# Optimization experiments

Measured on AMD Instinct MI355X. Metric: run time of the kernel, lower is better.

The kernel has to match this reference:

```python
import jax, jax.numpy as jnp
import numpy as np

N_NODES = 50000
N_EDGES = 800000
D_IN = 128
D_OUT = 128
BN_EPS = 1e-5


def setup_inputs() -> dict:
    key = jax.random.key(0)
    ks = jax.random.split(key, 8)
    node_feats = jax.random.normal(ks[0], (N_NODES, D_IN), dtype=jnp.float32)
    src = jax.random.randint(ks[1], (N_EDGES,), 0, N_NODES, dtype=jnp.int32)
    dst = jax.random.randint(ks[2], (N_EDGES,), 0, N_NODES, dtype=jnp.int32)
    # Glorot-ish init for weights
    scale = 1.0 / np.sqrt(D_IN)
    W = jax.random.normal(ks[3], (D_IN, D_OUT), dtype=jnp.float32) * scale
    b = jnp.zeros((D_OUT,), dtype=jnp.float32)
    Wr = jax.random.normal(ks[4], (D_IN, D_OUT), dtype=jnp.float32) * scale
    br = jnp.zeros((D_OUT,), dtype=jnp.float32)
    gamma = jnp.ones((D_OUT,), dtype=jnp.float32)
    beta = jnp.zeros((D_OUT,), dtype=jnp.float32)
    return {"node_feats": node_feats, "src": src, "dst": dst, "W": W, "b": b,
            "Wr": Wr, "br": br, "gamma": gamma, "beta": beta}


def reference(node_feats, src, dst, W, b, Wr, br, gamma, beta):
    N = node_feats.shape[0]
    ones_e = jnp.ones(src.shape[0], dtype=node_feats.dtype)
    # DGL GraphConv norm='both': D_out^{-1/2} on source side, D_in^{-1/2} on dest side
    deg_out = jnp.clip(jax.ops.segment_sum(ones_e, src, num_segments=N), 1.0)
    deg_in = jnp.clip(jax.ops.segment_sum(ones_e, dst, num_segments=N), 1.0)
    h = node_feats * jax.lax.rsqrt(deg_out)[:, None]        # [N, D_in]
    agg = jax.ops.segment_sum(h[src], dst, num_segments=N)  # gather + scatter-add, [N, D_in]
    agg = agg * jax.lax.rsqrt(deg_in)[:, None]
    gcn = jax.nn.relu(agg @ W + b)                           # GraphConv activation=relu
    res = jax.nn.relu(node_feats @ Wr + br)                  # residual branch
    y = gcn + res
    # BatchNorm1d (training mode: biased batch stats)
    mean = jnp.mean(y, axis=0)
    var = jnp.mean(jnp.square(y - mean), axis=0)
    out = (y - mean) * jax.lax.rsqrt(var + BN_EPS) * gamma + beta
    return out
```

## Files before the change

kernel.cpp:

```cpp
#include <hip/hip_runtime.h>

#define N_NODES 50000
#define N_EDGES 800000
#define D 128
#define BN_EPS 1e-5f
#define AGG_BLOCKS 2048
#define SCAN_BLOCKS 196
#define CHUNKS 64
#define EPC (N_EDGES / CHUNKS)
#define HALF_BINS 25600
#define HALF_U32 12800

typedef short bf16x8 __attribute__((ext_vector_type(8)));
typedef float f32x4  __attribute__((ext_vector_type(4)));
typedef unsigned int u32x4 __attribute__((ext_vector_type(4)));


__device__ __forceinline__ unsigned int pack_rne(float a, float b) {
    unsigned int ua = __float_as_uint(a); ua += 0x7fffu + ((ua >> 16) & 1u);
    unsigned int ub = __float_as_uint(b); ub += 0x7fffu + ((ub >> 16) & 1u);
    return (ua >> 16) | (ub & 0xffff0000u);
}
__device__ __forceinline__ unsigned short pack1_rne(float a) {
    unsigned int ua = __float_as_uint(a); ua += 0x7fffu + ((ua >> 16) & 1u);
    return (unsigned short)(ua >> 16);
}

__global__ __launch_bounds__(256) void hist_kernel(
        const int* __restrict__ dst, const int* __restrict__ src,
        unsigned int* __restrict__ histD, unsigned int* __restrict__ histS,
        const float* __restrict__ W, const float* __restrict__ Wr,
        uint4* __restrict__ pW, uint4* __restrict__ pWr) {
    __shared__ unsigned int h[HALF_U32];
    int tid = threadIdx.x;
    int c = blockIdx.x, r = blockIdx.y;
    if (c >= CHUNKS) {
        if (r != 0 || blockIdx.z != 0) return;
        int t = (c - CHUNKS) * 256 + tid;
        const float* S = (t & 2048) ? Wr : W;
        uint4* Dst     = (t & 2048) ? pWr : pW;
        int e = t & 2047;
        int lane = e & 63, ks = (e >> 6) & 3, ct = e >> 8;
        int n  = ct * 16 + (lane & 15);
        int k0 = ks * 32 + (lane >> 4) * 8;
        float v[8];
        #pragma unroll
        for (int j = 0; j < 8; j++) v[j] = S[(k0 + j) * D + n];
        uint4 rr;
        rr.x = pack_rne(v[0], v[1]); rr.y = pack_rne(v[2], v[3]);
        rr.z = pack_rne(v[4], v[5]); rr.w = pack_rne(v[6], v[7]);
        Dst[e] = rr;
        return;
    }
    const int* keys = blockIdx.z ? src : dst;
    unsigned int* hist = blockIdx.z ? histS : histD;
    for (int j = tid; j < HALF_U32; j += 256) h[j] = 0u;
    __syncthreads();
    int base = c * EPC;
    int lo = r * HALF_BINS;
    for (int i = tid; i < EPC; i += 256) {
        int b = keys[base + i] - lo;
        if ((unsigned)b < (unsigned)HALF_BINS)
            atomicAdd(&h[b >> 1], 1u << ((b & 1) * 16));
    }
    __syncthreads();
    unsigned int* out = hist + ((size_t)(r * CHUNKS + c)) * HALF_U32;
    for (int j = tid; j < HALF_U32; j += 256) out[j] = h[j];
}

__global__ __launch_bounds__(256) void merge_kernel(
        unsigned int* __restrict__ histD, unsigned int* __restrict__ histS,
        int* __restrict__ cnt_in, int* __restrict__ cnt_out) {
    int q = blockIdx.x * 256 + threadIdx.x;
    int r = blockIdx.y;
    unsigned int* hist = blockIdx.z ? histS : histD;
    int* cnt = blockIdx.z ? cnt_out : cnt_in;
    unsigned int lo = 0, hi = 0;
    for (int c = 0; c < CHUNKS; c++) {
        size_t idx = ((size_t)(r * CHUNKS + c)) * HALF_U32 + q;
        unsigned int v = hist[idx];
        hist[idx] = lo | (hi << 16);
        lo += v & 0xffffu; hi += v >> 16;
    }
    int n0 = r * HALF_BINS + q * 2;
    cnt[n0]     = (int)lo;
    cnt[n0 + 1] = (int)hi;
}

__global__ __launch_bounds__(256) void scan1_kernel(
        const int* __restrict__ cnt_in, int* __restrict__ row_ptr, int* __restrict__ blk_sum) {
    __shared__ int sh[256];
    int t = threadIdx.x;
    int i = blockIdx.x * 256 + t;
    int v = cnt_in[i];
    sh[t] = v;
    __syncthreads();
    int inc = v;
    #pragma unroll
    for (int off = 1; off < 256; off <<= 1) {
        int u = (t >= off) ? sh[t - off] : 0;
        __syncthreads();
        inc += u; sh[t] = inc;
        __syncthreads();
    }
    row_ptr[i] = inc - v;
    if (t == 255) blk_sum[blockIdx.x] = inc;
}

__global__ __launch_bounds__(256) void scan3_kernel(
        const int* __restrict__ cnt_in, const int* __restrict__ cnt_out,
        const int* __restrict__ blk_sum, int* __restrict__ row_ptr,
        float* __restrict__ rin, float* __restrict__ rout) {
    __shared__ int sh[256];
    int t = threadIdx.x;
    int v = (t < SCAN_BLOCKS) ? blk_sum[t] : 0;
    sh[t] = v;
    __syncthreads();
    int inc = v;
    #pragma unroll
    for (int off = 1; off < 256; off <<= 1) {
        int u = (t >= off) ? sh[t - off] : 0;
        __syncthreads();
        inc += u; sh[t] = inc;
        __syncthreads();
    }
    int boff = (blockIdx.x == 0) ? 0 : sh[blockIdx.x - 1];
    int i = blockIdx.x * 256 + t;
    if (i < N_NODES) {
        row_ptr[i] = row_ptr[i] + boff;
        int ci = cnt_in[i], co = cnt_out[i];
        rin[i]  = rsqrtf((float)(ci > 1 ? ci : 1));
        rout[i] = rsqrtf((float)(co > 1 ? co : 1));
    }
    if (blockIdx.x == SCAN_BLOCKS - 1 && t == 0) row_ptr[N_NODES] = N_EDGES;
}

__global__ __launch_bounds__(512) void fill2_kernel(
        const int* __restrict__ src, const int* __restrict__ dst,
        const int* __restrict__ row_ptr, const unsigned int* __restrict__ histP,
        int* __restrict__ csr_src) {
    __shared__ unsigned int h[HALF_U32];
    int tid = threadIdx.x;
    int c = blockIdx.x;
    int base = c * EPC;
    for (int r = 0; r < 2; r++) {
        for (int j = tid; j < HALF_U32; j += 512) h[j] = 0u;
        __syncthreads();
        int lo = r * HALF_BINS;
        const unsigned int* pre_c = histP + ((size_t)(r * CHUNKS + c)) * HALF_U32;
        for (int i = tid; i < EPC; i += 512) {
            int d = dst[base + i];
            int b = d - lo;
            if ((unsigned)b < (unsigned)HALF_BINS) {
                int sh = (b & 1) * 16;
                unsigned int old = atomicAdd(&h[b >> 1], 1u << sh);
                unsigned int rank = (old >> sh) & 0xffffu;
                unsigned int pre = (pre_c[b >> 1] >> sh) & 0xffffu;
                int p = row_ptr[d] + (int)(pre + rank);
                csr_src[p] = src[base + i];
            }
        }
        __syncthreads();
    }
}

__global__ __launch_bounds__(256) void gemm_mfma(
        const float* __restrict__ x, const uint4* __restrict__ pW,
        const uint4* __restrict__ pWr, const float* __restrict__ br,
        const float* __restrict__ rout, unsigned short* __restrict__ hwb,
        unsigned short* __restrict__ resb) {
    __shared__ unsigned short xs[64][136];
    int tid = threadIdx.x, wid = tid >> 6, lane = tid & 63;
    int quad = lane >> 4, l15 = lane & 15;
    int r0b = blockIdx.x * 64;
    const float4* xg = (const float4*)(x + (size_t)r0b * D);
    int maxidx = (N_NODES - r0b) * (D / 4);
    #pragma unroll
    for (int i = 0; i < 8; i++) {
        int idx = tid + 256 * i;
        float4 v = (idx < maxidx) ? xg[idx] : make_float4(0.f, 0.f, 0.f, 0.f);
        int row = idx >> 5, c0 = (idx & 31) * 4;
        *(unsigned int*)&xs[row][c0]     = pack_rne(v.x, v.y);
        *(unsigned int*)&xs[row][c0 + 2] = pack_rne(v.z, v.w);
    }
    __syncthreads();
    int wrow0 = wid * 16;
    bf16x8 A[4];
    #pragma unroll
    for (int ks = 0; ks < 4; ks++)
        A[ks] = *(const bf16x8*)&xs[wrow0 + l15][ks * 32 + quad * 8];
    f32x4 accW[8], accR[8];
    #pragma unroll
    for (int ct = 0; ct < 8; ct++) { accW[ct] = (f32x4)0.f; accR[ct] = (f32x4)0.f; }
    #pragma unroll
    for (int ct = 0; ct < 8; ct++) {
        #pragma unroll
        for (int ks = 0; ks < 4; ks++) {
            union { bf16x8 v; uint4 u; } Bw, Br2;
            Bw.u  = pW [(ct * 4 + ks) * 64 + lane];
            Br2.u = pWr[(ct * 4 + ks) * 64 + lane];
            accW[ct] = __builtin_amdgcn_mfma_f32_16x16x32_bf16(A[ks], Bw.v,  accW[ct], 0, 0, 0);
            accR[ct] = __builtin_amdgcn_mfma_f32_16x16x32_bf16(A[ks], Br2.v, accR[ct], 0, 0, 0);
        }
    }
    int r0 = r0b + wrow0;
    float ro[4]; int rowok[4];
    #pragma unroll
    for (int reg = 0; reg < 4; reg++) {
        int row = r0 + quad * 4 + reg;
        rowok[reg] = row < N_NODES;
        ro[reg] = rout[rowok[reg] ? row : N_NODES - 1];
    }
    #pragma unroll
    for (int ct = 0; ct < 8; ct++) {
        int c = ct * 16 + l15;
        float brv = br[c];
        #pragma unroll
        for (int reg = 0; reg < 4; reg++) {
            int row = r0 + quad * 4 + reg;
            if (rowok[reg]) {
                hwb [(size_t)row * D + c] = pack1_rne(accW[ct][reg] * ro[reg]);
                resb[(size_t)row * D + c] = pack1_rne(fmaxf(accR[ct][reg] + brv, 0.f));
            }
        }
    }
}

__device__ __forceinline__ float bf_lo(unsigned int v) { return __uint_as_float(v << 16); }
__device__ __forceinline__ float bf_hi(unsigned int v) { return __uint_as_float(v & 0xffff0000u); }

__device__ __forceinline__ void acc8(float* a, const uint4 v) {
    a[0] += bf_lo(v.x); a[1] += bf_hi(v.x);
    a[2] += bf_lo(v.y); a[3] += bf_hi(v.y);
    a[4] += bf_lo(v.z); a[5] += bf_hi(v.z);
    a[6] += bf_lo(v.w); a[7] += bf_hi(v.w);
}
__device__ __forceinline__ void acc8m(float* a, const uint4 v, float m) {
    a[0] = fmaf(m, bf_lo(v.x), a[0]); a[1] = fmaf(m, bf_hi(v.x), a[1]);
    a[2] = fmaf(m, bf_lo(v.y), a[2]); a[3] = fmaf(m, bf_hi(v.y), a[3]);
    a[4] = fmaf(m, bf_lo(v.z), a[4]); a[5] = fmaf(m, bf_hi(v.z), a[5]);
    a[6] = fmaf(m, bf_lo(v.w), a[6]); a[7] = fmaf(m, bf_hi(v.w), a[7]);
}

__device__ __forceinline__ int sel4(int qg, int i0, int i1, int i2, int i3) {
    int a = (qg & 1) ? i1 : i0;
    int b = (qg & 1) ? i3 : i2;
    return (qg & 2) ? b : a;
}

__device__ __forceinline__ void gather_accum(
        const unsigned int* __restrict__ hwb, int myidx, int cnt,
        int qg, int ql, float* a) {
    int i = 0;
    for (; i + 16 <= cnt; i += 16) {
        int p0 = sel4(qg, __builtin_amdgcn_readlane(myidx, i + 0),
                          __builtin_amdgcn_readlane(myidx, i + 1),
                          __builtin_amdgcn_readlane(myidx, i + 2),
                          __builtin_amdgcn_readlane(myidx, i + 3));
        int p1 = sel4(qg, __builtin_amdgcn_readlane(myidx, i + 4),
                          __builtin_amdgcn_readlane(myidx, i + 5),
                          __builtin_amdgcn_readlane(myidx, i + 6),
                          __builtin_amdgcn_readlane(myidx, i + 7));
        int p2 = sel4(qg, __builtin_amdgcn_readlane(myidx, i + 8),
                          __builtin_amdgcn_readlane(myidx, i + 9),
                          __builtin_amdgcn_readlane(myidx, i + 10),
                          __builtin_amdgcn_readlane(myidx, i + 11));
        int p3 = sel4(qg, __builtin_amdgcn_readlane(myidx, i + 12),
                          __builtin_amdgcn_readlane(myidx, i + 13),
                          __builtin_amdgcn_readlane(myidx, i + 14),
                          __builtin_amdgcn_readlane(myidx, i + 15));
        uint4 v0 = *((const uint4*)(hwb + (size_t)p0 * 64) + ql);
        uint4 v1 = *((const uint4*)(hwb + (size_t)p1 * 64) + ql);
        uint4 v2 = *((const uint4*)(hwb + (size_t)p2 * 64) + ql);
        uint4 v3 = *((const uint4*)(hwb + (size_t)p3 * 64) + ql);
        acc8(a, v0); acc8(a, v1); acc8(a, v2); acc8(a, v3);
    }
    for (; i + 4 <= cnt; i += 4) {
        int p0 = sel4(qg, __builtin_amdgcn_readlane(myidx, i + 0),
                          __builtin_amdgcn_readlane(myidx, i + 1),
                          __builtin_amdgcn_readlane(myidx, i + 2),
                          __builtin_amdgcn_readlane(myidx, i + 3));
        uint4 v0 = *((const uint4*)(hwb + (size_t)p0 * 64) + ql);
        acc8(a, v0);
    }
    int t = cnt - i;
    if (t > 0) {
        int lim = cnt - 1;
        int j1 = i + 1 <= lim ? i + 1 : lim;
        int j2 = i + 2 <= lim ? i + 2 : lim;
        int p0 = sel4(qg, __builtin_amdgcn_readlane(myidx, i),
                          __builtin_amdgcn_readlane(myidx, j1),
                          __builtin_amdgcn_readlane(myidx, j2),
                          __builtin_amdgcn_readlane(myidx, lim));
        uint4 v0 = *((const uint4*)(hwb + (size_t)p0 * 64) + ql);
        float m = (qg < t) ? 1.f : 0.f;
        acc8m(a, v0, m);
    }
}

__global__ __launch_bounds__(256) void agg_kernel(
        const unsigned int* __restrict__ hwb, const int* __restrict__ row_ptr,
        const int* __restrict__ csr_src, const float* __restrict__ rin,
        const float* __restrict__ bias, const unsigned short* __restrict__ resb,
        float* __restrict__ y, float* __restrict__ parts) {
    __shared__ float red[4 * 256];
    int tid = threadIdx.x;
    int lane = tid & 63, wid = tid >> 6;
    int wave = blockIdx.x * 4 + wid;
    int nw = AGG_BLOCKS * 4;
    int qg = lane >> 4;
    int ql = lane & 15;
    float s1[8] = {0,0,0,0,0,0,0,0}, s2[8] = {0,0,0,0,0,0,0,0};
    float4 bv0, bv1;
    if (lane < 16) {
        bv0 = ((const float4*)bias)[2 * lane];
        bv1 = ((const float4*)bias)[2 * lane + 1];
    }
    int n = wave;
    int e0 = 0, e1 = 0, mi = 0;
    u32x4 rv4 = (u32x4)0u;
    float ri = 0.f;
    if (n < N_NODES) {
        e0 = row_ptr[n]; e1 = row_ptr[n + 1];
        ri = rin[n];
        if (lane < 16) rv4 = __builtin_nontemporal_load((const u32x4*)(resb + (size_t)n * D) + lane);
        int c0 = e1 - e0; if (c0 > 64) c0 = 64;
        mi = (lane < c0) ? __builtin_nontemporal_load(csr_src + e0 + lane) : 0;
    }
    while (n < N_NODES) {
        int nn = n + nw;
        int ne0 = 0, ne1 = 0, nmi = 0;
        u32x4 nrv = (u32x4)0u;
        float nri = 0.f;
        if (nn < N_NODES) {
            ne0 = row_ptr[nn]; ne1 = row_ptr[nn + 1];
            nri = rin[nn];
            if (lane < 16) nrv = __builtin_nontemporal_load((const u32x4*)(resb + (size_t)nn * D) + lane);
            int nc = ne1 - ne0; if (nc > 64) nc = 64;
            nmi = (lane < nc) ? __builtin_nontemporal_load(csr_src + ne0 + lane) : 0;
        }
        float a[8] = {0,0,0,0,0,0,0,0};
        {
            int cnt = e1 - e0; if (cnt > 64) cnt = 64;
            gather_accum(hwb, mi, cnt, qg, ql, a);
        }
        for (int j0 = e0 + 64; j0 < e1; j0 += 64) {
            int cnt = e1 - j0; if (cnt > 64) cnt = 64;
            int mw = (lane < cnt) ? __builtin_nontemporal_load(csr_src + j0 + lane) : 0;
            gather_accum(hwb, mw, cnt, qg, ql, a);
        }
        #pragma unroll
        for (int k = 0; k < 8; k++) {
            a[k] += __shfl_xor(a[k], 16);
            a[k] += __shfl_xor(a[k], 32);
        }
        if (lane < 16) {
            float o[8];
            o[0] = fmaxf(a[0] * ri + bv0.x, 0.f) + bf_lo(rv4.x);
            o[1] = fmaxf(a[1] * ri + bv0.y, 0.f) + bf_hi(rv4.x);
            o[2] = fmaxf(a[2] * ri + bv0.z, 0.f) + bf_lo(rv4.y);
            o[3] = fmaxf(a[3] * ri + bv0.w, 0.f) + bf_hi(rv4.y);
            o[4] = fmaxf(a[4] * ri + bv1.x, 0.f) + bf_lo(rv4.z);
            o[5] = fmaxf(a[5] * ri + bv1.y, 0.f) + bf_hi(rv4.z);
            o[6] = fmaxf(a[6] * ri + bv1.z, 0.f) + bf_lo(rv4.w);
            o[7] = fmaxf(a[7] * ri + bv1.w, 0.f) + bf_hi(rv4.w);
            float4* yv = (float4*)(y + (size_t)n * D);
            yv[2 * lane]     = make_float4(o[0], o[1], o[2], o[3]);
            yv[2 * lane + 1] = make_float4(o[4], o[5], o[6], o[7]);
            #pragma unroll
            for (int k = 0; k < 8; k++) { s1[k] += o[k]; s2[k] += o[k] * o[k]; }
        }
        n = nn; e0 = ne0; e1 = ne1; mi = nmi; rv4 = nrv; ri = nri;
    }
    if (lane < 16) {
        int c0 = lane * 8;
        #pragma unroll
        for (int k = 0; k < 8; k++) {
            red[wid * 256 + c0 + k]       = s1[k];
            red[wid * 256 + 128 + c0 + k] = s2[k];
        }
    }
    __syncthreads();
    if (tid < 256) {
        float v = red[tid] + red[256 + tid] + red[512 + tid] + red[768 + tid];
        parts[(size_t)blockIdx.x * 256 + tid] = v;
    }
}

__global__ __launch_bounds__(256) void bn_fin2(
        const float* __restrict__ parts, const float* __restrict__ gamma,
        const float* __restrict__ beta, float* __restrict__ scsh) {
    __shared__ float rs1[256], rs2[256];
    int c = blockIdx.x, t = threadIdx.x;
    float s1 = 0.f, s2 = 0.f;
    for (int b = t; b < AGG_BLOCKS; b += 256) {
        s1 += parts[(size_t)b * 256 + c];
        s2 += parts[(size_t)b * 256 + 128 + c];
    }
    rs1[t] = s1; rs2[t] = s2;
    __syncthreads();
    for (int off = 128; off > 0; off >>= 1) {
        if (t < off) { rs1[t] += rs1[t + off]; rs2[t] += rs2[t + off]; }
        __syncthreads();
    }
    if (t == 0) {
        const float invN = 1.0f / (float)N_NODES;
        float mean = rs1[0] * invN;
        float var  = rs2[0] * invN - mean * mean;
        float sc = gamma[c] * rsqrtf(var + BN_EPS);
        scsh[c] = sc;
        scsh[128 + c] = beta[c] - mean * sc;
    }
}

__global__ void norm_kernel(float* __restrict__ y, const float* __restrict__ scsh) {
    int i = blockIdx.x * blockDim.x + threadIdx.x;
    if (i < N_NODES * 32) {
        float4 v = ((float4*)y)[i];
        int c = (i & 31) * 4;
        v.x = v.x * scsh[c]     + scsh[128 + c];
        v.y = v.y * scsh[c + 1] + scsh[128 + c + 1];
        v.z = v.z * scsh[c + 2] + scsh[128 + c + 2];
        v.w = v.w * scsh[c + 3] + scsh[128 + c + 3];
        ((float4*)y)[i] = v;
    }
}

extern "C" void kernel_launch(void* const* d_in, const int* in_sizes, int n_in,
                              void* d_out, int out_size, void* d_ws, size_t ws_size,
                              hipStream_t stream) {
    const float* x     = (const float*)d_in[0];
    const int*   src   = (const int*)d_in[1];
    const int*   dst   = (const int*)d_in[2];
    const float* W     = (const float*)d_in[3];
    const float* b     = (const float*)d_in[4];
    const float* Wr    = (const float*)d_in[5];
    const float* br    = (const float*)d_in[6];
    const float* gamma = (const float*)d_in[7];
    const float* beta  = (const float*)d_in[8];
    float* out = (float*)d_out;

    char* ws = (char*)d_ws;
    int*   cnt_in  = (int*)(ws + 0);
    int*   cnt_out = (int*)(ws + 262144);
    int*   row_ptr = (int*)(ws + 524288);
    float* rin     = (float*)(ws + 1048576);
    float* rout    = (float*)(ws + 1310720);
    float* scsh    = (float*)(ws + 1576960);
    int*   blk_sum = (int*)(ws + 1579008);
    int*   csr_src = (int*)(ws + 1581056);
    unsigned short* hwb = (unsigned short*)(ws + 4800000);
    float* parts   = (float*)(ws + 17600000);
    uint4* pW      = (uint4*)(ws + 19697152);
    uint4* pWr     = (uint4*)(ws + 19729920);
    unsigned int* histD = (unsigned int*)(ws + 19762688);
    unsigned int* histS = (unsigned int*)(ws + 26316288);
    unsigned short* resb = (unsigned short*)(ws + 19762688);

    hist_kernel<<<dim3(CHUNKS + 16, 2, 2), 256, 0, stream>>>(dst, src, histD, histS, W, Wr, pW, pWr);
    merge_kernel<<<dim3(HALF_U32 / 256, 2, 2), 256, 0, stream>>>(histD, histS, cnt_in, cnt_out);
    scan1_kernel<<<SCAN_BLOCKS, 256, 0, stream>>>(cnt_in, row_ptr, blk_sum);
    scan3_kernel<<<SCAN_BLOCKS, 256, 0, stream>>>(cnt_in, cnt_out, blk_sum, row_ptr, rin, rout);
    fill2_kernel<<<CHUNKS, 512, 0, stream>>>(src, dst, row_ptr, histD, csr_src);
    gemm_mfma<<<(N_NODES + 63) / 64, 256, 0, stream>>>(x, pW, pWr, br, rout, hwb, resb);
    agg_kernel<<<AGG_BLOCKS, 256, 0, stream>>>((const unsigned int*)hwb, row_ptr, csr_src, rin, b, resb, out, parts);
    bn_fin2<<<128, 256, 0, stream>>>(parts, gamma, beta, scsh);
    norm_kernel<<<(N_NODES * 32 + 255) / 256, 256, 0, stream>>>(out, scsh);
}
```

Before: 239.0 us.

## Store gathered features in FP8, bf16 pre-norm output, and parallelize CSR fill

New measurement: 219.7 us. -8.1%, faster.

```diff
diff --git a/kernel.cpp b/kernel.cpp
--- a/kernel.cpp
+++ b/kernel.cpp
@@ -13,6 +13,7 @@
 
 typedef short bf16x8 __attribute__((ext_vector_type(8)));
 typedef float f32x4  __attribute__((ext_vector_type(4)));
+typedef float f32x2  __attribute__((ext_vector_type(2)));
 typedef unsigned int u32x4 __attribute__((ext_vector_type(4)));
 
 
@@ -24,6 +25,10 @@
 __device__ __forceinline__ unsigned short pack1_rne(float a) {
     unsigned int ua = __float_as_uint(a); ua += 0x7fffu + ((ua >> 16) & 1u);
     return (unsigned short)(ua >> 16);
+}
+__device__ __forceinline__ unsigned char pack1_fp8(float a) {
+    unsigned int u = __builtin_amdgcn_cvt_pk_fp8_f32(a, a, 0, false);
+    return (unsigned char)(u & 0xffu);
 }
 
 __global__ __launch_bounds__(256) void hist_kernel(
@@ -141,33 +146,30 @@
         int* __restrict__ csr_src) {
     __shared__ unsigned int h[HALF_U32];
     int tid = threadIdx.x;
-    int c = blockIdx.x;
+    int c = blockIdx.x, r = blockIdx.y;
     int base = c * EPC;
-    for (int r = 0; r < 2; r++) {
-        for (int j = tid; j < HALF_U32; j += 512) h[j] = 0u;
-        __syncthreads();
-        int lo = r * HALF_BINS;
-        const unsigned int* pre_c = histP + ((size_t)(r * CHUNKS + c)) * HALF_U32;
-        for (int i = tid; i < EPC; i += 512) {
-            int d = dst[base + i];
-            int b = d - lo;
-            if ((unsigned)b < (unsigned)HALF_BINS) {
-                int sh = (b & 1) * 16;
-                unsigned int old = atomicAdd(&h[b >> 1], 1u << sh);
-                unsigned int rank = (old >> sh) & 0xffffu;
-                unsigned int pre = (pre_c[b >> 1] >> sh) & 0xffffu;
-                int p = row_ptr[d] + (int)(pre + rank);
-                csr_src[p] = src[base + i];
-            }
-        }
-        __syncthreads();
+    for (int j = tid; j < HALF_U32; j += 512) h[j] = 0u;
+    __syncthreads();
+    int lo = r * HALF_BINS;
+    const unsigned int* pre_c = histP + ((size_t)(r * CHUNKS + c)) * HALF_U32;
+    for (int i = tid; i < EPC; i += 512) {
+        int d = dst[base + i];
+        int b = d - lo;
+        if ((unsigned)b < (unsigned)HALF_BINS) {
+            int sh = (b & 1) * 16;
+            unsigned int old = atomicAdd(&h[b >> 1], 1u << sh);
+            unsigned int rank = (old >> sh) & 0xffffu;
+            unsigned int pre = (pre_c[b >> 1] >> sh) & 0xffffu;
+            int p = row_ptr[d] + (int)(pre + rank);
+            csr_src[p] = src[base + i];
+        }
     }
 }
 
 __global__ __launch_bounds__(256) void gemm_mfma(
         const float* __restrict__ x, const uint4* __restrict__ pW,
         const uint4* __restrict__ pWr, const float* __restrict__ br,
-        const float* __restrict__ rout, unsigned short* __restrict__ hwb,
+        const float* __restrict__ rout, unsigned char* __restrict__ hwb8,
         unsigned short* __restrict__ resb) {
     __shared__ unsigned short xs[64][136];
     int tid = threadIdx.x, wid = tid >> 6, lane = tid & 63;
@@ -219,7 +221,7 @@
         for (int reg = 0; reg < 4; reg++) {
             int row = r0 + quad * 4 + reg;
             if (rowok[reg]) {
-                hwb [(size_t)row * D + c] = pack1_rne(accW[ct][reg] * ro[reg]);
+                hwb8[(size_t)row * D + c] = pack1_fp8(accW[ct][reg] * ro[reg]);
                 resb[(size_t)row * D + c] = pack1_rne(fmaxf(accR[ct][reg] + brv, 0.f));
             }
         }
@@ -229,17 +231,23 @@
 __device__ __forceinline__ float bf_lo(unsigned int v) { return __uint_as_float(v << 16); }
 __device__ __forceinline__ float bf_hi(unsigned int v) { return __uint_as_float(v & 0xffff0000u); }
 
-__device__ __forceinline__ void acc8(float* a, const uint4 v) {
-    a[0] += bf_lo(v.x); a[1] += bf_hi(v.x);
-    a[2] += bf_lo(v.y); a[3] += bf_hi(v.y);
-    a[4] += bf_lo(v.z); a[5] += bf_hi(v.z);
-    a[6] += bf_lo(v.w); a[7] += bf_hi(v.w);
-}
-__device__ __forceinline__ void acc8m(float* a, const uint4 v, float m) {
-    a[0] = fmaf(m, bf_lo(v.x), a[0]); a[1] = fmaf(m, bf_hi(v.x), a[1]);
-    a[2] = fmaf(m, bf_lo(v.y), a[2]); a[3] = fmaf(m, bf_hi(v.y), a[3]);
-    a[4] = fmaf(m, bf_lo(v.z), a[4]); a[5] = fmaf(m, bf_hi(v.z), a[5]);
-    a[6] = fmaf(m, bf_lo(v.w), a[6]); a[7] = fmaf(m, bf_hi(v.w), a[7]);
+__device__ __forceinline__ void acc8f8(float* a, const uint2 v) {
+    f32x2 p0 = __builtin_amdgcn_cvt_pk_f32_fp8(v.x, false);
+    f32x2 p1 = __builtin_amdgcn_cvt_pk_f32_fp8(v.x, true);
+    f32x2 p2 = __builtin_amdgcn_cvt_pk_f32_fp8(v.y, false);
+    f32x2 p3 = __builtin_amdgcn_cvt_pk_f32_fp8(v.y, true);
+    a[0] += p0.x; a[1] += p0.y; a[2] += p1.x; a[3] += p1.y;
+    a[4] += p2.x; a[5] += p2.y; a[6] += p3.x; a[7] += p3.y;
+}
+__device__ __forceinline__ void acc8f8m(float* a, const uint2 v, float m) {
+    f32x2 p0 = __builtin_amdgcn_cvt_pk_f32_fp8(v.x, false);
+    f32x2 p1 = __builtin_amdgcn_cvt_pk_f32_fp8(v.x, true);
+    f32x2 p2 = __builtin_amdgcn_cvt_pk_f32_fp8(v.y, false);
+    f32x2 p3 = __builtin_amdgcn_cvt_pk_f32_fp8(v.y, true);
+    a[0] = fmaf(m, p0.x, a[0]); a[1] = fmaf(m, p0.y, a[1]);
+    a[2] = fmaf(m, p1.x, a[2]); a[3] = fmaf(m, p1.y, a[3]);
+    a[4] = fmaf(m, p2.x, a[4]); a[5] = fmaf(m, p2.y, a[5]);
+    a[6] = fmaf(m, p3.x, a[6]); a[7] = fmaf(m, p3.y, a[7]);
 }
 
 __device__ __forceinline__ int sel4(int qg, int i0, int i1, int i2, int i3) {
@@ -249,7 +257,7 @@
 }
 
 __device__ __forceinline__ void gather_accum(
-        const unsigned int* __restrict__ hwb, int myidx, int cnt,
+        const unsigned char* __restrict__ hwb8, int myidx, int cnt,
         int qg, int ql, float* a) {
     int i = 0;
     for (; i + 16 <= cnt; i += 16) {
@@ -269,19 +277,19 @@
                           __builtin_amdgcn_readlane(myidx, i + 13),
                           __builtin_amdgcn_readlane(myidx, i + 14),
                           __builtin_amdgcn_readlane(myidx, i + 15));
-        uint4 v0 = *((const uint4*)(hwb + (size_t)p0 * 64) + ql);
-        uint4 v1 = *((const uint4*)(hwb + (size_t)p1 * 64) + ql);
-        uint4 v2 = *((const uint4*)(hwb + (size_t)p2 * 64) + ql);
-        uint4 v3 = *((const uint4*)(hwb + (size_t)p3 * 64) + ql);
-        acc8(a, v0); acc8(a, v1); acc8(a, v2); acc8(a, v3);
+        uint2 v0 = *((const uint2*)(hwb8 + (size_t)p0 * 128) + ql);
+        uint2 v1 = *((const uint2*)(hwb8 + (size_t)p1 * 128) + ql);
+        uint2 v2 = *((const uint2*)(hwb8 + (size_t)p2 * 128) + ql);
+        uint2 v3 = *((const uint2*)(hwb8 + (size_t)p3 * 128) + ql);
+        acc8f8(a, v0); acc8f8(a, v1); acc8f8(a, v2); acc8f8(a, v3);
     }
     for (; i + 4 <= cnt; i += 4) {
         int p0 = sel4(qg, __builtin_amdgcn_readlane(myidx, i + 0),
                           __builtin_amdgcn_readlane(myidx, i + 1),
                           __builtin_amdgcn_readlane(myidx, i + 2),
                           __builtin_amdgcn_readlane(myidx, i + 3));
-        uint4 v0 = *((const uint4*)(hwb + (size_t)p0 * 64) + ql);
-        acc8(a, v0);
+        uint2 v0 = *((const uint2*)(hwb8 + (size_t)p0 * 128) + ql);
+        acc8f8(a, v0);
     }
     int t = cnt - i;
     if (t > 0) {
@@ -292,17 +300,17 @@
                           __builtin_amdgcn_readlane(myidx, j1),
                           __builtin_amdgcn_readlane(myidx, j2),
                           __builtin_amdgcn_readlane(myidx, lim));
-        uint4 v0 = *((const uint4*)(hwb + (size_t)p0 * 64) + ql);
+        uint2 v0 = *((const uint2*)(hwb8 + (size_t)p0 * 128) + ql);
         float m = (qg < t) ? 1.f : 0.f;
-        acc8m(a, v0, m);
+        acc8f8m(a, v0, m);
     }
 }
 
 __global__ __launch_bounds__(256) void agg_kernel(
-        const unsigned int* __restrict__ hwb, const int* __restrict__ row_ptr,
+        const unsigned char* __restrict__ hwb8, const int* __restrict__ row_ptr,
         const int* __restrict__ csr_src, const float* __restrict__ rin,
         const float* __restrict__ bias, const unsigned short* __restrict__ resb,
-        float* __restrict__ y, float* __restrict__ parts) {
+        unsigned short* __restrict__ yb, float* __restrict__ parts) {
     __shared__ float red[4 * 256];
     int tid = threadIdx.x;
     int lane = tid & 63, wid = tid >> 6;
@@ -342,12 +350,12 @@
         float a[8] = {0,0,0,0,0,0,0,0};
         {
             int cnt = e1 - e0; if (cnt > 64) cnt = 64;
-            gather_accum(hwb, mi, cnt, qg, ql, a);
+            gather_accum(hwb8, mi, cnt, qg, ql, a);
         }
         for (int j0 = e0 + 64; j0 < e1; j0 += 64) {
             int cnt = e1 - j0; if (cnt > 64) cnt = 64;
             int mw = (lane < cnt) ? __builtin_nontemporal_load(csr_src + j0 + lane) : 0;
-            gather_accum(hwb, mw, cnt, qg, ql, a);
+            gather_accum(hwb8, mw, cnt, qg, ql, a);
         }
         #pragma unroll
         for (int k = 0; k < 8; k++) {
@@ -364,9 +372,10 @@
             o[5] = fmaxf(a[5] * ri + bv1.y, 0.f) + bf_hi(rv4.z);
             o[6] = fmaxf(a[6] * ri + bv1.z, 0.f) + bf_lo(rv4.w);
             o[7] = fmaxf(a[7] * ri + bv1.w, 0.f) + bf_hi(rv4.w);
-            float4* yv = (float4*)(y + (size_t)n * D);
-            yv[2 * lane]     = make_float4(o[0], o[1], o[2], o[3]);
-            yv[2 * lane + 1] = make_float4(o[4], o[5], o[6], o[7]);
+            uint4 w;
+            w.x = pack_rne(o[0], o[1]); w.y = pack_rne(o[2], o[3]);
+            w.z = pack_rne(o[4], o[5]); w.w = pack_rne(o[6], o[7]);
+            *((uint4*)(yb + (size_t)n * D) + lane) = w;
             #pragma unroll
             for (int k = 0; k < 8; k++) { s1[k] += o[k]; s2[k] += o[k] * o[k]; }
         }
@@ -413,16 +422,23 @@
     }
 }
 
-__global__ void norm_kernel(float* __restrict__ y, const float* __restrict__ scsh) {
+__global__ void norm_kernel(const unsigned short* __restrict__ yb,
+                            const float* __restrict__ scsh, float* __restrict__ out) {
     int i = blockIdx.x * blockDim.x + threadIdx.x;
-    if (i < N_NODES * 32) {
-        float4 v = ((float4*)y)[i];
-        int c = (i & 31) * 4;
-        v.x = v.x * scsh[c]     + scsh[128 + c];
-        v.y = v.y * scsh[c + 1] + scsh[128 + c + 1];
-        v.z = v.z * scsh[c + 2] + scsh[128 + c + 2];
-        v.w = v.w * scsh[c + 3] + scsh[128 + c + 3];
-        ((float4*)y)[i] = v;
+    if (i < N_NODES * 16) {
+        uint4 v = ((const uint4*)yb)[i];
+        int c = (i & 15) * 8;
+        float4 o0, o1;
+        o0.x = bf_lo(v.x) * scsh[c]     + scsh[128 + c];
+        o0.y = bf_hi(v.x) * scsh[c + 1] + scsh[128 + c + 1];
+        o0.z = bf_lo(v.y) * scsh[c + 2] + scsh[128 + c + 2];
+        o0.w = bf_hi(v.y) * scsh[c + 3] + scsh[128 + c + 3];
+        o1.x = bf_lo(v.z) * scsh[c + 4] + scsh[128 + c + 4];
+        o1.y = bf_hi(v.z) * scsh[c + 5] + scsh[128 + c + 5];
+        o1.z = bf_lo(v.w) * scsh[c + 6] + scsh[128 + c + 6];
+        o1.w = bf_hi(v.w) * scsh[c + 7] + scsh[128 + c + 7];
+        float4* ov = (float4*)out + (size_t)i * 2;
+        ov[0] = o0; ov[1] = o1;
     }
 }
 
@@ -444,26 +460,27 @@
     int*   cnt_in  = (int*)(ws + 0);
     int*   cnt_out = (int*)(ws + 262144);
     int*   row_ptr = (int*)(ws + 524288);
-    float* rin     = (float*)(ws + 1048576);
-    float* rout    = (float*)(ws + 1310720);
-    float* scsh    = (float*)(ws + 1576960);
-    int*   blk_sum = (int*)(ws + 1579008);
-    int*   csr_src = (int*)(ws + 1581056);
-    unsigned short* hwb = (unsigned short*)(ws + 4800000);
-    float* parts   = (float*)(ws + 17600000);
-    uint4* pW      = (uint4*)(ws + 19697152);
-    uint4* pWr     = (uint4*)(ws + 19729920);
-    unsigned int* histD = (unsigned int*)(ws + 19762688);
-    unsigned int* histS = (unsigned int*)(ws + 26316288);
-    unsigned short* resb = (unsigned short*)(ws + 19762688);
+    float* rin     = (float*)(ws + 786432);
+    float* rout    = (float*)(ws + 1048576);
+    float* scsh    = (float*)(ws + 1310720);
+    int*   blk_sum = (int*)(ws + 1312768);
+    int*   csr_src = (int*)(ws + 1576960);
+    unsigned char*  hwb8 = (unsigned char*)(ws + 4800000);
+    unsigned short* resb = (unsigned short*)(ws + 11200000);
+    unsigned short* yb   = (unsigned short*)(ws + 24000000);
+    float* parts   = (float*)(ws + 36800000);
+    uint4* pW      = (uint4*)(ws + 38897152);
+    uint4* pWr     = (uint4*)(ws + 38929920);
+    unsigned int* histD = (unsigned int*)(ws + 38962688);
+    unsigned int* histS = (unsigned int*)(ws + 45516288);
 
     hist_kernel<<<dim3(CHUNKS + 16, 2, 2), 256, 0, stream>>>(dst, src, histD, histS, W, Wr, pW, pWr);
     merge_kernel<<<dim3(HALF_U32 / 256, 2, 2), 256, 0, stream>>>(histD, histS, cnt_in, cnt_out);
     scan1_kernel<<<SCAN_BLOCKS, 256, 0, stream>>>(cnt_in, row_ptr, blk_sum);
     scan3_kernel<<<SCAN_BLOCKS, 256, 0, stream>>>(cnt_in, cnt_out, blk_sum, row_ptr, rin, rout);
-    fill2_kernel<<<CHUNKS, 512, 0, stream>>>(src, dst, row_ptr, histD, csr_src);
-    gemm_mfma<<<(N_NODES + 63) / 64, 256, 0, stream>>>(x, pW, pWr, br, rout, hwb, resb);
-    agg_kernel<<<AGG_BLOCKS, 256, 0, stream>>>((const unsigned int*)hwb, row_ptr, csr_src, rin, b, resb, out, parts);
+    fill2_kernel<<<dim3(CHUNKS, 2), 512, 0, stream>>>(src, dst, row_ptr, histD, csr_src);
+    gemm_mfma<<<(N_NODES + 63) / 64, 256, 0, stream>>>(x, pW, pWr, br, rout, hwb8, resb);
+    agg_kernel<<<AGG_BLOCKS, 256, 0, stream>>>(hwb8, row_ptr, csr_src, rin, b, resb, yb, parts);
     bn_fin2<<<128, 256, 0, stream>>>(parts, gamma, beta, scsh);
-    norm_kernel<<<(N_NODES * 32 + 255) / 256, 256, 0, stream>>>(out, scsh);
-}
+    norm_kernel<<<(N_NODES * 16 + 255) / 256, 256, 0, stream>>>(yb, scsh, out);
+}
```
